# Optimization experiments

Hardware: AMD Instinct MI355X
Metric: run time of the kernel (lower is better)

Reference implementation:

```python
import jax, jax.numpy as jnp
import numpy as np

N_NODES = 100000
FEAT = 256
HID = 256
BATCH = 512
NUM_SAMPLES = [25, 10]  # layer_infos[0].num_samples, layer_infos[1].num_samples


def setup_inputs() -> dict:
    key = jax.random.key(0)
    ks = jax.random.split(key, 7)
    scale = 0.05
    return {
        "features": jax.random.normal(ks[0], (N_NODES, FEAT), dtype=jnp.float32),
        "adj": jax.random.randint(ks[1], (N_NODES, NUM_SAMPLES[0]), 0, N_NODES, dtype=jnp.int32),
        "batch": jax.random.randint(ks[2], (BATCH,), 0, N_NODES, dtype=jnp.int32),
        "W_self_0": jax.random.normal(ks[3], (FEAT, HID), dtype=jnp.float32) * scale,
        "W_neigh_0": jax.random.normal(ks[4], (FEAT, HID), dtype=jnp.float32) * scale,
        "W_self_1": jax.random.normal(ks[5], (HID, HID), dtype=jnp.float32) * scale,
        "W_neigh_1": jax.random.normal(ks[6], (HID, HID), dtype=jnp.float32) * scale,
    }


def reference(features, adj, batch, W_self_0, W_neigh_0, W_self_1, W_neigh_1):
    B = batch.shape[0]
    n_layers = 2
    # --- sample(): reverse-order neighbor expansion (deterministic: first-k slots) ---
    # hop 1 uses layer_infos[-1].num_samples = 10, hop 2 uses layer_infos[0].num_samples = 25
    s1 = adj[batch][:, : NUM_SAMPLES[1]].reshape(-1)  # [B*10]
    s2 = adj[s1][:, : NUM_SAMPLES[0]].reshape(-1)     # [B*250]
    support = [1, NUM_SAMPLES[1], NUM_SAMPLES[1] * NUM_SAMPLES[0]]  # [1, 10, 250]
    # --- gather input features per hop (irregular gather, memory bound) ---
    hidden = [features[batch], features[s1], features[s2]]
    Ws = [(W_self_0, W_neigh_0), (W_self_1, W_neigh_1)]
    for layer in range(n_layers):
        act = jax.nn.relu if layer < n_layers - 1 else (lambda x: x)
        W_s, W_n = Ws[layer]
        next_hidden = []
        for hop in range(n_layers - layer):
            n_smp = NUM_SAMPLES[n_layers - hop - 1]
            self_vecs = hidden[hop]  # [B*support[hop], d]
            neigh = hidden[hop + 1].reshape(B * support[hop], n_smp, -1)
            neigh_mean = neigh.mean(axis=1)  # mean aggregator
            # concat=False -> sum of self and neighbor transforms
            next_hidden.append(act(self_vecs @ W_s + neigh_mean @ W_n))
        hidden = next_hidden
    out = hidden[0]  # [B, HID]
    # GraphSAGE l2-normalizes final embeddings
    norm = jnp.maximum(jnp.linalg.norm(out, axis=1, keepdims=True), 1e-12)
    return out / norm
```

## Files before the change

kernel.cpp:

```cpp
#include <hip/hip_runtime.h>
#include <cstdint>
#include <cstddef>

#define NNODES 100000
#define FEATD  256
#define HIDD   256
#define NBATCH 512
#define FAN1   10
#define FAN2   25
#define NS1    (NBATCH*FAN1)
#define MTOT   (NBATCH+NS1)

typedef __attribute__((ext_vector_type(8))) short short8;
typedef __attribute__((ext_vector_type(4))) float f32x4;

__device__ __forceinline__ unsigned short f2bf(float f) {
    unsigned int u = __float_as_uint(f);
    unsigned int r = (u + 0x7fffu + ((u >> 16) & 1u)) >> 16;
    return (unsigned short)r;
}
__device__ __forceinline__ float bf2f(unsigned short h) {
    return __uint_as_float(((unsigned int)h) << 16);
}

__global__ __launch_bounds__(256) void k_prep(
    const float* __restrict__ Ws0, const float* __restrict__ Wn0,
    const float* __restrict__ Ws1, const float* __restrict__ Wn1,
    const int* __restrict__ adj, const int* __restrict__ batch,
    unsigned short* __restrict__ B0t, unsigned short* __restrict__ B1t,
    int* __restrict__ s1, int* __restrict__ s2) {
    const int t = threadIdx.x;
    if (blockIdx.x < 64) {
        __shared__ unsigned short Ts[64][72];
        const int which = blockIdx.x >> 5;
        const int loc   = blockIdx.x & 31;
        const int kt = loc >> 2, nt = loc & 3;
        const int k0 = kt * 64, n0 = nt * 64;
        const float* W;
        if (which == 0)
            W = (k0 < 256) ? (Ws0 + (size_t)k0 * 256) : (Wn0 + (size_t)(k0 - 256) * 256);
        else
            W = (k0 < 256) ? (Ws1 + (size_t)k0 * 256) : (Wn1 + (size_t)(k0 - 256) * 256);
        unsigned short* Bt = which ? B1t : B0t;
        #pragma unroll
        for (int i = 0; i < 4; ++i) {
            int s  = t + i * 256;
            int kr = s >> 4;
            int c4 = s & 15;
            float4 v = *reinterpret_cast<const float4*>(W + (size_t)kr * 256 + n0 + c4 * 4);
            Ts[c4 * 4 + 0][kr] = f2bf(v.x);
            Ts[c4 * 4 + 1][kr] = f2bf(v.y);
            Ts[c4 * 4 + 2][kr] = f2bf(v.z);
            Ts[c4 * 4 + 3][kr] = f2bf(v.w);
        }
        __syncthreads();
        #pragma unroll
        for (int i = 0; i < 2; ++i) {
            int s  = t + i * 256;
            int nl = s >> 3;
            int k8 = (s & 7) * 8;
            *reinterpret_cast<short8*>(Bt + (size_t)(n0 + nl) * 512 + k0 + k8) =
                *reinterpret_cast<const short8*>(&Ts[nl][k8]);
        }
        return;
    }
    __shared__ int hs[FAN1];
    const int b  = blockIdx.x - 64;
    const int nb = batch[b];
    if (t < FAN1) {
        int v = adj[(size_t)nb * FAN2 + t];
        s1[b * FAN1 + t] = v;
        hs[t] = v;
    }
    __syncthreads();
    if (t < FAN1 * FAN2) {
        const int u = t / FAN2, v = t - u * FAN2;
        s2[(size_t)(b * FAN1 + u) * FAN2 + v] = adj[(size_t)hs[u] * FAN2 + v];
    }
}

template<int FAN>
__device__ __forceinline__ void gather4(
    const float* __restrict__ feat, const int* nidx, const int* node,
    int l, int wv, unsigned short (*As)[520]) {
    static_assert(FAN % 5 == 0, "FAN must be a multiple of 5");
    constexpr int BPR = FAN / 5;
    constexpr int NB4 = 4 * BPR;
    float4 sv0 = *reinterpret_cast<const float4*>(feat + (size_t)node[0] * FEATD + l * 4);
    float4 sv1 = *reinterpret_cast<const float4*>(feat + (size_t)node[1] * FEATD + l * 4);
    float4 sv2 = *reinterpret_cast<const float4*>(feat + (size_t)node[2] * FEATD + l * 4);
    float4 sv3 = *reinterpret_cast<const float4*>(feat + (size_t)node[3] * FEATD + l * 4);
#define GLD(ROW, K) (*reinterpret_cast<const float4*>( \
        feat + (size_t)__shfl(nidx[ROW], (K)) * FEATD + l * 4))
    float4 c0, c1, c2, c3, c4, n0, n1, n2, n3, n4;
    c0 = GLD(0, 0); c1 = GLD(0, 1); c2 = GLD(0, 2); c3 = GLD(0, 3); c4 = GLD(0, 4);
    float4 a = make_float4(0.f, 0.f, 0.f, 0.f);
    #pragma unroll
    for (int g = 0; g < NB4; ++g) {
        const int row = g / BPR;
        if (g + 1 < NB4) {
            const int nr = (g + 1) / BPR;
            const int nk = ((g + 1) % BPR) * 5;
            n0 = GLD(nr, nk + 0); n1 = GLD(nr, nk + 1); n2 = GLD(nr, nk + 2);
            n3 = GLD(nr, nk + 3); n4 = GLD(nr, nk + 4);
        }
        a.x += (c0.x + c1.x) + (c2.x + c3.x) + c4.x;
        a.y += (c0.y + c1.y) + (c2.y + c3.y) + c4.y;
        a.z += (c0.z + c1.z) + (c2.z + c3.z) + c4.z;
        a.w += (c0.w + c1.w) + (c2.w + c3.w) + c4.w;
        if ((g + 1) % BPR == 0) {
            const float s = 1.0f / (float)FAN;
            float4 sv = (row == 0) ? sv0 : (row == 1) ? sv1 : (row == 2) ? sv2 : sv3;
            ushort4 ps, pn;
            ps.x = f2bf(sv.x);      ps.y = f2bf(sv.y);
            ps.z = f2bf(sv.z);      ps.w = f2bf(sv.w);
            pn.x = f2bf(a.x * s);   pn.y = f2bf(a.y * s);
            pn.z = f2bf(a.z * s);   pn.w = f2bf(a.w * s);
            const int r = wv * 4 + row;
            *reinterpret_cast<ushort4*>(&As[r][l * 4])       = ps;
            *reinterpret_cast<ushort4*>(&As[r][256 + l * 4]) = pn;
            a = make_float4(0.f, 0.f, 0.f, 0.f);
        }
        if (g + 1 < NB4) { c0 = n0; c1 = n1; c2 = n2; c3 = n3; c4 = n4; }
    }
#undef GLD
}

__global__ __launch_bounds__(256) void k_gg0(
    const float* __restrict__ feat, const int* __restrict__ batch,
    const int* __restrict__ s1, const int* __restrict__ s2,
    const unsigned short* __restrict__ B0t,
    unsigned short* __restrict__ H0, unsigned short* __restrict__ H1) {
    __shared__ __align__(16) unsigned short As[16][520];
    const int t   = threadIdx.x;
    const int wv  = t >> 6;
    const int l   = t & 63;
    const int q   = l >> 4;
    const int m15 = l & 15;
    const int r0  = blockIdx.x * 16;
    const bool isBatch = (r0 < NBATCH);

    int node[4], nidx[4];
    #pragma unroll
    for (int i = 0; i < 4; ++i) {
        const int R = r0 + wv * 4 + i;
        if (isBatch) {
            node[i] = batch[R];
            nidx[i] = (l < FAN1) ? s1[R * FAN1 + l] : 0;
        } else {
            const int idx = R - NBATCH;
            node[i] = s1[idx];
            nidx[i] = (l < FAN2) ? s2[(size_t)idx * FAN2 + l] : 0;
        }
    }
    if (isBatch) gather4<FAN1>(feat, nidx, node, l, wv, As);
    else         gather4<FAN2>(feat, nidx, node, l, wv, As);
    __syncthreads();

    f32x4 acc0 = (f32x4)0.f, acc1 = (f32x4)0.f, acc2 = (f32x4)0.f, acc3 = (f32x4)0.f;
    const unsigned short* b0p = B0t + (size_t)(wv * 64 +  0 + m15) * 512;
    const unsigned short* b1p = B0t + (size_t)(wv * 64 + 16 + m15) * 512;
    const unsigned short* b2p = B0t + (size_t)(wv * 64 + 32 + m15) * 512;
    const unsigned short* b3p = B0t + (size_t)(wv * 64 + 48 + m15) * 512;
    #pragma unroll
    for (int kt = 0; kt < 16; ++kt) {
        const int kk = kt * 32 + q * 8;
        short8 a  = *reinterpret_cast<const short8*>(&As[m15][kk]);
        short8 b0 = *reinterpret_cast<const short8*>(b0p + kk);
        short8 b1 = *reinterpret_cast<const short8*>(b1p + kk);
        short8 b2 = *reinterpret_cast<const short8*>(b2p + kk);
        short8 b3 = *reinterpret_cast<const short8*>(b3p + kk);
        acc0 = __builtin_amdgcn_mfma_f32_16x16x32_bf16(a, b0, acc0, 0, 0, 0);
        acc1 = __builtin_amdgcn_mfma_f32_16x16x32_bf16(a, b1, acc1, 0, 0, 0);
        acc2 = __builtin_amdgcn_mfma_f32_16x16x32_bf16(a, b2, acc2, 0, 0, 0);
        acc3 = __builtin_amdgcn_mfma_f32_16x16x32_bf16(a, b3, acc3, 0, 0, 0);
    }

    #pragma unroll
    for (int f = 0; f < 4; ++f) {
        const int n = wv * 64 + f * 16 + m15;
        const f32x4& a = (f == 0) ? acc0 : (f == 1) ? acc1 : (f == 2) ? acc2 : acc3;
        #pragma unroll
        for (int j = 0; j < 4; ++j) {
            int m = r0 + q * 4 + j;
            unsigned short v = f2bf(fmaxf(a[j], 0.f));
            if (isBatch)
                H0[(size_t)m * HIDD + n] = v;
            else
                H1[(size_t)(m - NBATCH) * HIDD + n] = v;
        }
    }
}

__global__ __launch_bounds__(512) void k_l1(
    const unsigned short* __restrict__ H0, const unsigned short* __restrict__ H1,
    const unsigned short* __restrict__ B1t, float* __restrict__ out) {
    __shared__ __align__(16) unsigned short As[16][520];
    __shared__ float rn[16][8];
    const int t   = threadIdx.x;
    const int wv  = t >> 6;
    const int l   = t & 63;
    const int q   = l >> 4;
    const int m15 = l & 15;
    const int rb  = blockIdx.x * 16;

    {
        int r = t >> 5, c8 = (t & 31) * 8;
        *reinterpret_cast<short8*>(&As[r][c8]) =
            *reinterpret_cast<const short8*>(H0 + (size_t)(rb + r) * HIDD + c8);
    }
    {
        int r = t >> 5, c8 = (t & 31) * 8;
        const unsigned short* base = H1 + (size_t)(rb + r) * FAN1 * HIDD + c8;
        float a[8];
        #pragma unroll
        for (int e = 0; e < 8; ++e) a[e] = 0.f;
        #pragma unroll
        for (int j = 0; j < FAN1; ++j) {
            short8 v = *reinterpret_cast<const short8*>(base + (size_t)j * HIDD);
            #pragma unroll
            for (int e = 0; e < 8; ++e) a[e] += bf2f((unsigned short)v[e]);
        }
        short8 p;
        #pragma unroll
        for (int e = 0; e < 8; ++e) p[e] = (short)f2bf(a[e] * (1.0f / FAN1));
        *reinterpret_cast<short8*>(&As[r][256 + c8]) = p;
    }
    __syncthreads();

    f32x4 acc0 = (f32x4)0.f, acc1 = (f32x4)0.f;
    const unsigned short* b0p = B1t + (size_t)(wv * 32 + m15) * 512;
    const unsigned short* b1p = B1t + (size_t)(wv * 32 + 16 + m15) * 512;
    #pragma unroll
    for (int kt = 0; kt < 8; ++kt) {
        const int kb = kt * 64;
        #pragma unroll
        for (int s2i = 0; s2i < 2; ++s2i) {
            const int kk = kb + s2i * 32 + q * 8;
            short8 a  = *reinterpret_cast<const short8*>(&As[m15][kk]);
            short8 b0 = *reinterpret_cast<const short8*>(b0p + kk);
            short8 b1 = *reinterpret_cast<const short8*>(b1p + kk);
            acc0 = __builtin_amdgcn_mfma_f32_16x16x32_bf16(a, b0, acc0, 0, 0, 0);
            acc1 = __builtin_amdgcn_mfma_f32_16x16x32_bf16(a, b1, acc1, 0, 0, 0);
        }
    }

    #pragma unroll
    for (int j = 0; j < 4; ++j) {
        float p = acc0[j] * acc0[j] + acc1[j] * acc1[j];
        p += __shfl_xor(p, 1);
        p += __shfl_xor(p, 2);
        p += __shfl_xor(p, 4);
        p += __shfl_xor(p, 8);
        if (m15 == 0) rn[q * 4 + j][wv] = p;
    }
    __syncthreads();

    #pragma unroll
    for (int j = 0; j < 4; ++j) {
        const int m = q * 4 + j;
        float s = rn[m][0] + rn[m][1] + rn[m][2] + rn[m][3]
                + rn[m][4] + rn[m][5] + rn[m][6] + rn[m][7];
        float inv = 1.0f / fmaxf(sqrtf(s), 1e-12f);
        out[(size_t)(rb + m) * HIDD + wv * 32 + m15]      = acc0[j] * inv;
        out[(size_t)(rb + m) * HIDD + wv * 32 + 16 + m15] = acc1[j] * inv;
    }
}

extern "C" void kernel_launch(void* const* d_in, const int* in_sizes, int n_in,
                              void* d_out, int out_size, void* d_ws, size_t ws_size,
                              hipStream_t stream) {
    const float* feat  = (const float*)d_in[0];
    const int*   adj   = (const int*)d_in[1];
    const int*   batch = (const int*)d_in[2];
    const float* Ws0   = (const float*)d_in[3];
    const float* Wn0   = (const float*)d_in[4];
    const float* Ws1   = (const float*)d_in[5];
    const float* Wn1   = (const float*)d_in[6];
    float* out = (float*)d_out;

    char* ws = (char*)d_ws;
    unsigned short* B0t = (unsigned short*)(ws + 0);
    unsigned short* B1t = (unsigned short*)(ws + 262144);
    unsigned short* H0  = (unsigned short*)(ws + 524288);
    unsigned short* H1  = (unsigned short*)(ws + 786432);
    int*            s1  = (int*)(ws + 3407872);
    int*            s2  = (int*)(ws + 3428352);

    k_prep<<<64 + NBATCH, 256, 0, stream>>>(Ws0, Wn0, Ws1, Wn1, adj, batch,
                                            B0t, B1t, s1, s2);
    k_gg0<<<MTOT / 16, 256, 0, stream>>>(feat, batch, s1, s2, B0t, H0, H1);
    k_l1<<<NBATCH / 16, 512, 0, stream>>>(H0, H1, B1t, out);
}
```

Baseline: 193.0 us.

## Gather one row per wave with 8-row blocks of 512 threads in k_gg0

```diff
diff --git a/kernel.cpp b/kernel.cpp
--- a/kernel.cpp
+++ b/kernel.cpp
@@ -80,53 +80,41 @@
 }
 
 template<int FAN>
-__device__ __forceinline__ void gather4(
-    const float* __restrict__ feat, const int* nidx, const int* node,
-    int l, int wv, unsigned short (*As)[520]) {
+__device__ __forceinline__ void gather_row(
+    const float* __restrict__ feat, int nidx, int node,
+    int l, int row, unsigned short (*As)[520]) {
     static_assert(FAN % 5 == 0, "FAN must be a multiple of 5");
-    constexpr int BPR = FAN / 5;
-    constexpr int NB4 = 4 * BPR;
-    float4 sv0 = *reinterpret_cast<const float4*>(feat + (size_t)node[0] * FEATD + l * 4);
-    float4 sv1 = *reinterpret_cast<const float4*>(feat + (size_t)node[1] * FEATD + l * 4);
-    float4 sv2 = *reinterpret_cast<const float4*>(feat + (size_t)node[2] * FEATD + l * 4);
-    float4 sv3 = *reinterpret_cast<const float4*>(feat + (size_t)node[3] * FEATD + l * 4);
-#define GLD(ROW, K) (*reinterpret_cast<const float4*>( \
-        feat + (size_t)__shfl(nidx[ROW], (K)) * FEATD + l * 4))
+    float4 sv = *reinterpret_cast<const float4*>(feat + (size_t)node * FEATD + l * 4);
+#define GLD(K) (*reinterpret_cast<const float4*>( \
+        feat + (size_t)__shfl(nidx, (K)) * FEATD + l * 4))
     float4 c0, c1, c2, c3, c4, n0, n1, n2, n3, n4;
-    c0 = GLD(0, 0); c1 = GLD(0, 1); c2 = GLD(0, 2); c3 = GLD(0, 3); c4 = GLD(0, 4);
+    c0 = GLD(0); c1 = GLD(1); c2 = GLD(2); c3 = GLD(3); c4 = GLD(4);
     float4 a = make_float4(0.f, 0.f, 0.f, 0.f);
-    #pragma unroll
-    for (int g = 0; g < NB4; ++g) {
-        const int row = g / BPR;
-        if (g + 1 < NB4) {
-            const int nr = (g + 1) / BPR;
-            const int nk = ((g + 1) % BPR) * 5;
-            n0 = GLD(nr, nk + 0); n1 = GLD(nr, nk + 1); n2 = GLD(nr, nk + 2);
-            n3 = GLD(nr, nk + 3); n4 = GLD(nr, nk + 4);
+    constexpr int NB = FAN / 5;
+    #pragma unroll
+    for (int g = 0; g < NB; ++g) {
+        if (g + 1 < NB) {
+            n0 = GLD(5*g+5); n1 = GLD(5*g+6); n2 = GLD(5*g+7);
+            n3 = GLD(5*g+8); n4 = GLD(5*g+9);
         }
         a.x += (c0.x + c1.x) + (c2.x + c3.x) + c4.x;
         a.y += (c0.y + c1.y) + (c2.y + c3.y) + c4.y;
         a.z += (c0.z + c1.z) + (c2.z + c3.z) + c4.z;
         a.w += (c0.w + c1.w) + (c2.w + c3.w) + c4.w;
-        if ((g + 1) % BPR == 0) {
-            const float s = 1.0f / (float)FAN;
-            float4 sv = (row == 0) ? sv0 : (row == 1) ? sv1 : (row == 2) ? sv2 : sv3;
-            ushort4 ps, pn;
-            ps.x = f2bf(sv.x);      ps.y = f2bf(sv.y);
-            ps.z = f2bf(sv.z);      ps.w = f2bf(sv.w);
-            pn.x = f2bf(a.x * s);   pn.y = f2bf(a.y * s);
-            pn.z = f2bf(a.z * s);   pn.w = f2bf(a.w * s);
-            const int r = wv * 4 + row;
-            *reinterpret_cast<ushort4*>(&As[r][l * 4])       = ps;
-            *reinterpret_cast<ushort4*>(&As[r][256 + l * 4]) = pn;
-            a = make_float4(0.f, 0.f, 0.f, 0.f);
-        }
-        if (g + 1 < NB4) { c0 = n0; c1 = n1; c2 = n2; c3 = n3; c4 = n4; }
+        if (g + 1 < NB) { c0 = n0; c1 = n1; c2 = n2; c3 = n3; c4 = n4; }
     }
 #undef GLD
-}
-
-__global__ __launch_bounds__(256) void k_gg0(
+    const float s = 1.0f / (float)FAN;
+    ushort4 ps, pn;
+    ps.x = f2bf(sv.x);      ps.y = f2bf(sv.y);
+    ps.z = f2bf(sv.z);      ps.w = f2bf(sv.w);
+    pn.x = f2bf(a.x * s);   pn.y = f2bf(a.y * s);
+    pn.z = f2bf(a.z * s);   pn.w = f2bf(a.w * s);
+    *reinterpret_cast<ushort4*>(&As[row][l * 4])       = ps;
+    *reinterpret_cast<ushort4*>(&As[row][256 + l * 4]) = pn;
+}
+
+__global__ __launch_bounds__(512, 4) void k_gg0(
     const float* __restrict__ feat, const int* __restrict__ batch,
     const int* __restrict__ s1, const int* __restrict__ s2,
     const unsigned short* __restrict__ B0t,
@@ -137,57 +125,53 @@
     const int l   = t & 63;
     const int q   = l >> 4;
     const int m15 = l & 15;
-    const int r0  = blockIdx.x * 16;
+    const int r0  = blockIdx.x * 8;
     const bool isBatch = (r0 < NBATCH);
 
-    int node[4], nidx[4];
-    #pragma unroll
-    for (int i = 0; i < 4; ++i) {
-        const int R = r0 + wv * 4 + i;
-        if (isBatch) {
-            node[i] = batch[R];
-            nidx[i] = (l < FAN1) ? s1[R * FAN1 + l] : 0;
-        } else {
-            const int idx = R - NBATCH;
-            node[i] = s1[idx];
-            nidx[i] = (l < FAN2) ? s2[(size_t)idx * FAN2 + l] : 0;
-        }
-    }
-    if (isBatch) gather4<FAN1>(feat, nidx, node, l, wv, As);
-    else         gather4<FAN2>(feat, nidx, node, l, wv, As);
-    __syncthreads();
-
-    f32x4 acc0 = (f32x4)0.f, acc1 = (f32x4)0.f, acc2 = (f32x4)0.f, acc3 = (f32x4)0.f;
-    const unsigned short* b0p = B0t + (size_t)(wv * 64 +  0 + m15) * 512;
-    const unsigned short* b1p = B0t + (size_t)(wv * 64 + 16 + m15) * 512;
-    const unsigned short* b2p = B0t + (size_t)(wv * 64 + 32 + m15) * 512;
-    const unsigned short* b3p = B0t + (size_t)(wv * 64 + 48 + m15) * 512;
+    *reinterpret_cast<short8*>(&As[8 + wv][l * 8]) = (short8)0;
+
+    const int R = r0 + wv;
+    int node, nidx;
+    if (isBatch) {
+        node = batch[R];
+        nidx = (l < FAN1) ? s1[R * FAN1 + l] : 0;
+    } else {
+        const int idx = R - NBATCH;
+        node = s1[idx];
+        nidx = (l < FAN2) ? s2[(size_t)idx * FAN2 + l] : 0;
+    }
+    if (isBatch) gather_row<FAN1>(feat, nidx, node, l, wv, As);
+    else         gather_row<FAN2>(feat, nidx, node, l, wv, As);
+    __syncthreads();
+
+    f32x4 acc0 = (f32x4)0.f, acc1 = (f32x4)0.f;
+    const unsigned short* b0p = B0t + (size_t)(wv * 32 +  0 + m15) * 512;
+    const unsigned short* b1p = B0t + (size_t)(wv * 32 + 16 + m15) * 512;
     #pragma unroll
     for (int kt = 0; kt < 16; ++kt) {
         const int kk = kt * 32 + q * 8;
         short8 a  = *reinterpret_cast<const short8*>(&As[m15][kk]);
         short8 b0 = *reinterpret_cast<const short8*>(b0p + kk);
         short8 b1 = *reinterpret_cast<const short8*>(b1p + kk);
-        short8 b2 = *reinterpret_cast<const short8*>(b2p + kk);
-        short8 b3 = *reinterpret_cast<const short8*>(b3p + kk);
         acc0 = __builtin_amdgcn_mfma_f32_16x16x32_bf16(a, b0, acc0, 0, 0, 0);
         acc1 = __builtin_amdgcn_mfma_f32_16x16x32_bf16(a, b1, acc1, 0, 0, 0);
-        acc2 = __builtin_amdgcn_mfma_f32_16x16x32_bf16(a, b2, acc2, 0, 0, 0);
-        acc3 = __builtin_amdgcn_mfma_f32_16x16x32_bf16(a, b3, acc3, 0, 0, 0);
-    }
-
-    #pragma unroll
-    for (int f = 0; f < 4; ++f) {
-        const int n = wv * 64 + f * 16 + m15;
-        const f32x4& a = (f == 0) ? acc0 : (f == 1) ? acc1 : (f == 2) ? acc2 : acc3;
+    }
+
+    #pragma unroll
+    for (int f = 0; f < 2; ++f) {
+        const int n = wv * 32 + f * 16 + m15;
+        const f32x4& a = f ? acc1 : acc0;
         #pragma unroll
         for (int j = 0; j < 4; ++j) {
-            int m = r0 + q * 4 + j;
-            unsigned short v = f2bf(fmaxf(a[j], 0.f));
-            if (isBatch)
-                H0[(size_t)m * HIDD + n] = v;
-            else
-                H1[(size_t)(m - NBATCH) * HIDD + n] = v;
+            const int ml = q * 4 + j;
+            if (ml < 8) {
+                const int m = r0 + ml;
+                unsigned short v = f2bf(fmaxf(a[j], 0.f));
+                if (isBatch)
+                    H0[(size_t)m * HIDD + n] = v;
+                else
+                    H1[(size_t)(m - NBATCH) * HIDD + n] = v;
+            }
         }
     }
 }
@@ -289,6 +273,6 @@
 
     k_prep<<<64 + NBATCH, 256, 0, stream>>>(Ws0, Wn0, Ws1, Wn1, adj, batch,
                                             B0t, B1t, s1, s2);
-    k_gg0<<<MTOT / 16, 256, 0, stream>>>(feat, batch, s1, s2, B0t, H0, H1);
+    k_gg0<<<MTOT / 8, 512, 0, stream>>>(feat, batch, s1, s2, B0t, H0, H1);
     k_l1<<<NBATCH / 16, 512, 0, stream>>>(H0, H1, B1t, out);
 }
```

New measurement: 196.0 us. Within noise of the previous version (+1.6%).
